# Optimization experiments

Hardware: AMD Instinct MI355X
Metric: run time of the kernel (lower is better)

Reference implementation:

```python
import jax, jax.numpy as jnp
import numpy as np

N_NODES = 50000
N_EDGES = 800000
F_IN = 11
HID = 128
N_ACT = 6


def _gcn_conv(x, W, b, src, dst, n):
    # PyG GCNConv: x' = D^{-1/2}(A+I)D^{-1/2} (x W) + b, with self-loops.
    h = x @ W  # [N, H]
    ones = jnp.ones(src.shape[0], dtype=h.dtype)
    deg = jax.ops.segment_sum(ones, dst, num_segments=n) + 1.0  # +1 self-loop
    dinv = jax.lax.rsqrt(deg)
    enorm = dinv[src] * dinv[dst]  # [E]
    msg = h[src] * enorm[:, None]  # gather + scale
    agg = jax.ops.segment_sum(msg, dst, num_segments=n)
    agg = agg + h * (dinv * dinv)[:, None]  # self-loop contribution (norm = 1/deg)
    return agg + b


def _mlp2(x, W1, b1, W2, b2):
    return jax.nn.relu(x @ W1 + b1) @ W2 + b2


def setup_inputs() -> dict:
    key = jax.random.key(0)
    ks = jax.random.split(key, 16)
    def g(k, shape, scale):
        return jax.random.normal(k, shape, dtype=jnp.float32) * scale
    x = g(ks[0], (N_NODES, F_IN), 1.0)
    edge_index = jax.random.randint(ks[1], (2, N_EDGES), 0, N_NODES, dtype=jnp.int64)
    return {
        "x": x,
        "edge_index": edge_index,
        "W1": g(ks[2], (F_IN, HID), 1.0 / np.sqrt(F_IN)),
        "b1": jnp.zeros((HID,), jnp.float32),
        "W2": g(ks[3], (HID, HID), 1.0 / np.sqrt(HID)),
        "b2": jnp.zeros((HID,), jnp.float32),
        "W3": g(ks[4], (HID, HID), 1.0 / np.sqrt(HID)),
        "b3": jnp.zeros((HID,), jnp.float32),
        "Wv1": g(ks[5], (HID, HID), 1.0 / np.sqrt(HID)),
        "bv1": jnp.zeros((HID,), jnp.float32),
        "Wv2": g(ks[6], (HID, 1), 1.0 / np.sqrt(HID)),
        "bv2": jnp.zeros((1,), jnp.float32),
        "Wa1": g(ks[7], (HID, HID), 1.0 / np.sqrt(HID)),
        "ba1": jnp.zeros((HID,), jnp.float32),
        "Wa2": g(ks[8], (HID, N_ACT), 1.0 / np.sqrt(HID)),
        "ba2": jnp.zeros((N_ACT,), jnp.float32),
    }


def reference(x, edge_index, W1, b1, W2, b2, W3, b3,
              Wv1, bv1, Wv2, bv2, Wa1, ba1, Wa2, ba2):
    src, dst = edge_index[0], edge_index[1]
    n = x.shape[0]
    h = jax.nn.relu(_gcn_conv(x, W1, b1, src, dst, n))
    h = jax.nn.relu(_gcn_conv(h, W2, b2, src, dst, n))
    h = jax.nn.relu(_gcn_conv(h, W3, b3, src, dst, n))
    # global_mean_pool with batch = zeros -> single-graph mean over nodes
    g = jnp.mean(h, axis=0, keepdims=True)  # [1, HID]
    value = _mlp2(g, Wv1, bv1, Wv2, bv2)          # [1, 1]
    advantage = _mlp2(g, Wa1, ba1, Wa2, ba2)      # [1, N_ACT]
    q = value + (advantage - jnp.mean(advantage, axis=-1, keepdims=True))
    return q
```

## Files before the change

kernel.cpp:

```cpp
#include <hip/hip_runtime.h>

#define HID 128
#define F_IN 11
#define FP 16
#define N_ACT 6
#define EPB 2048
#define LMAX 6144
#define CAP 8192

typedef __bf16 bf16;
typedef __bf16 v8bf __attribute__((ext_vector_type(8)));
typedef float f32x4 __attribute__((ext_vector_type(4)));
typedef float v2f __attribute__((ext_vector_type(2)));

__device__ inline float lo16(unsigned u) { return __uint_as_float(u << 16); }
__device__ inline float hi16(unsigned u) { return __uint_as_float(u & 0xffff0000u); }
__device__ inline unsigned pk2(float a, float b) {
  union { bf16 h; unsigned short u; } x, y;
  x.h = (bf16)a; y.h = (bf16)b;
  return ((unsigned)y.u << 16) | x.u;
}
__device__ inline v2f fp8_dec_lo(unsigned v) {
  return __builtin_amdgcn_cvt_pk_f32_fp8(v, false);
}
__device__ inline v2f fp8_dec_hi(unsigned v) {
  return __builtin_amdgcn_cvt_pk_f32_fp8(v, true);
}
__device__ inline unsigned fp8_enc2_lo(float a, float b, unsigned old) {
  return __builtin_amdgcn_cvt_pk_fp8_f32(a, b, old, false);
}
__device__ inline unsigned fp8_enc2_hi(float a, float b, unsigned old) {
  return __builtin_amdgcn_cvt_pk_fp8_f32(a, b, old, true);
}
__device__ inline unsigned char fp8_enc1(float v) {
  return (unsigned char)(__builtin_amdgcn_cvt_pk_fp8_f32(v, v, 0u, false) & 0xffu);
}


__global__ __launch_bounds__(256) void k_init(int* __restrict__ gcur,
                                              float* __restrict__ gsum, int nbkt) {
  int t = threadIdx.x;
  if (t < nbkt) gcur[t] = t * CAP;
  if (t < HID) gsum[t] = 0.f;
}

__global__ __launch_bounds__(256) void k_part(const int* __restrict__ esrc,
                                              const int* __restrict__ edst,
                                              int* __restrict__ gcur,
                                              unsigned* __restrict__ ebuf,
                                              const float* __restrict__ W2,
                                              const float* __restrict__ W3,
                                              bf16* __restrict__ WT2,
                                              bf16* __restrict__ WT3,
                                              int E, int nbkt) {
  __shared__ int hist[256], lofs[256], lcur[256], gbase[256];
  __shared__ unsigned sbuf[EPB];
  int t = threadIdx.x;
  hist[t] = 0;
  if (blockIdx.x < 64) {
    int i = blockIdx.x * 256 + t;
    int nn = i >> 7, k = i & 127;
    WT2[i] = (bf16)W2[k * 128 + nn];
    WT3[i] = (bf16)W3[k * 128 + nn];
  }
  __syncthreads();
  int start = blockIdx.x * EPB, end = min(E, start + EPB);
  unsigned u[8];
#pragma unroll
  for (int i = 0; i < 8; ++i) {
    int e = start + t + i * 256;
    if (e < end) {
      int s = esrc[e], d = edst[e];
      u[i] = ((unsigned)d << 16) | (unsigned)s;
      atomicAdd(&hist[d >> 8], 1);
    }
  }
  __syncthreads();
  int h = hist[t];
  lofs[t] = h;
  __syncthreads();
  for (int off = 1; off < 256; off <<= 1) {
    int x = (t >= off) ? lofs[t - off] : 0;
    __syncthreads();
    lofs[t] += x;
    __syncthreads();
  }
  lcur[t] = lofs[t] - h;
  if (t < nbkt && h) gbase[t] = atomicAdd(&gcur[t], h);
  __syncthreads();
#pragma unroll
  for (int i = 0; i < 8; ++i) {
    int e = start + t + i * 256;
    if (e < end) {
      int b = (int)(u[i] >> 24);
      int p = atomicAdd(&lcur[b], 1);
      sbuf[p] = u[i];
    }
  }
  __syncthreads();
  int m = end - start;
  for (int i = t; i < m; i += 256) {
    unsigned v = sbuf[i];
    int b = (int)(v >> 24);
    int excl = lofs[b] - hist[b];
    ebuf[gbase[b] + (i - excl)] = v;
  }
}

__global__ __launch_bounds__(256) void k_local(const unsigned* __restrict__ ebuf,
                                               const int* __restrict__ gcur,
                                               int2* __restrict__ rbe,
                                               float* __restrict__ dinv,
                                               unsigned short* __restrict__ cs,
                                               const float* __restrict__ x,
                                               bf16* __restrict__ xs, int n) {
  __shared__ int hist[256], lofs[256], cur[256];
  __shared__ float dsh[256];
  __shared__ unsigned sb[LMAX];
  int b = blockIdx.x, t = threadIdx.x;
  int rb = b * CAP, re = gcur[b];
  int m = re - rb;
  int nbase = b << 8;
  bool fit = (m <= LMAX);
  hist[t] = 0;
  __syncthreads();
  if (fit) {
    for (int i = t; i < m; i += 256) {
      unsigned u = ebuf[rb + i];
      sb[i] = u;
      atomicAdd(&hist[(int)(u >> 16) - nbase], 1);
    }
  } else {
    for (int i = t; i < m; i += 256)
      atomicAdd(&hist[(int)(ebuf[rb + i] >> 16) - nbase], 1);
  }
  __syncthreads();
  int h = hist[t];
  lofs[t] = h;
  __syncthreads();
  for (int off = 1; off < 256; off <<= 1) {
    int v = (t >= off) ? lofs[t - off] : 0;
    __syncthreads();
    lofs[t] += v;
    __syncthreads();
  }
  int excl = lofs[t] - h;
  cur[t] = rb + excl;
  float dv = rsqrtf((float)h + 1.0f);
  dsh[t] = dv;
  int g = nbase + t;
  if (g < n) {
    rbe[g] = make_int2(rb + excl, rb + lofs[t]);
    dinv[g] = dv;
  }
  __syncthreads();
  if (fit) {
    for (int i = t; i < m; i += 256) {
      unsigned u = sb[i];
      int p = atomicAdd(&cur[(int)(u >> 16) - nbase], 1);
      cs[p] = (unsigned short)(u & 0xffffu);
    }
  } else {
    for (int i = t; i < m; i += 256) {
      unsigned u = ebuf[rb + i];
      int p = atomicAdd(&cur[(int)(u >> 16) - nbase], 1);
      cs[p] = (unsigned short)(u & 0xffffu);
    }
  }
  for (int i = t; i < 256 * FP; i += 256) {
    int node = nbase + (i >> 4), c = i & 15;
    if (node < n)
      xs[(size_t)node * FP + c] =
          (bf16)((c < F_IN) ? x[(size_t)node * F_IN + c] * dsh[i >> 4] : 0.f);
  }
}


__global__ __launch_bounds__(256) void k_layer1(const bf16* __restrict__ xs,
                                                const float* __restrict__ dinv,
                                                const int2* __restrict__ rbe,
                                                const unsigned short* __restrict__ cs,
                                                const float* __restrict__ W1,
                                                const float* __restrict__ b1,
                                                unsigned* __restrict__ H8, int n) {
  __shared__ float Ws[F_IN * HID];
  __shared__ float A1s[64][17];
  int tid = threadIdx.x;
  int n0 = blockIdx.x * 64;
  for (int i = tid; i < F_IN * HID; i += 256) Ws[i] = W1[i];
  int wave = tid >> 6, lane = tid & 63;
  int g8 = lane >> 3, c = lane & 7;
  const unsigned* xs2 = (const unsigned*)xs;
#pragma unroll
  for (int r = 0; r < 2; ++r) {
    int row = wave * 16 + r * 8 + g8;
    int node = n0 + row;
    unsigned sv = 0;
    int j = 0, jend = 0;
    float dd = 0.f;
    if (node < n) {
      sv = xs2[(size_t)node * 8 + c];
      int2 be = rbe[node];
      j = be.x; jend = be.y;
      dd = dinv[node];
    }
    float ax = lo16(sv), ay = hi16(sv);
    for (; j < jend; j += 4) {
#pragma unroll
      for (int k = 0; k < 4; ++k) {
        int jj = j + k;
        bool ok = jj < jend;
        int sidx = cs[ok ? jj : jend - 1];
        unsigned v = xs2[(size_t)sidx * 8 + c];
        float mm = ok ? 1.f : 0.f;
        ax = fmaf(lo16(v), mm, ax);
        ay = fmaf(hi16(v), mm, ay);
      }
    }
    A1s[row][c * 2] = ax * dd;
    A1s[row][c * 2 + 1] = ay * dd;
  }
  __syncthreads();
  int tc = tid & 15, tr = tid >> 4;
  float bb[8];
#pragma unroll
  for (int j = 0; j < 8; ++j) bb[j] = b1[tc * 8 + j];
#pragma unroll
  for (int i = 0; i < 4; ++i) {
    int row = tr * 4 + i;
    int node = n0 + row;
    if (node >= n) continue;
    float acc[8];
#pragma unroll
    for (int j = 0; j < 8; ++j) acc[j] = 0.f;
#pragma unroll
    for (int k = 0; k < F_IN; ++k) {
      float xk = A1s[row][k];
      const float* wr = &Ws[k * HID + tc * 8];
#pragma unroll
      for (int j = 0; j < 8; ++j) acc[j] = fmaf(xk, wr[j], acc[j]);
    }
    float dd = dinv[node];
    float o[8];
#pragma unroll
    for (int j = 0; j < 8; ++j) o[j] = fmaxf(acc[j] + bb[j], 0.f) * dd;
    unsigned w0 = 0, w1 = 0;
    w0 = fp8_enc2_lo(o[0], o[1], w0);
    w0 = fp8_enc2_hi(o[2], o[3], w0);
    w1 = fp8_enc2_lo(o[4], o[5], w1);
    w1 = fp8_enc2_hi(o[6], o[7], w1);
    ((uint2*)H8)[(size_t)node * 16 + tc] = make_uint2(w0, w1);
  }
}


__global__ __launch_bounds__(256) void k_gather(const unsigned* __restrict__ tab,
                                                const float* __restrict__ dinv,
                                                const int2* __restrict__ rbe,
                                                const unsigned short* __restrict__ cs,
                                                bf16* __restrict__ A, int n, int nbx) {
  int bid = blockIdx.x;
  int slice = bid / nbx;
  int bx = bid - slice * nbx;
  int t = threadIdx.x;
  int node = bx * 16 + (t >> 4);
  int c = t & 15;
  int soff = slice * 16;
  if (node >= n) return;
  unsigned sv = tab[(size_t)node * 32 + soff + c];
  v2f slo = fp8_dec_lo(sv), shi = fp8_dec_hi(sv);
  float a0 = slo.x, a1 = slo.y, a2 = shi.x, a3 = shi.y;
  int2 be = rbe[node];
  int j = be.x, jend = be.y;
  for (; j < jend; j += 8) {
#pragma unroll
    for (int k = 0; k < 8; ++k) {
      int jj = j + k;
      bool ok = jj < jend;
      int sidx = cs[ok ? jj : jend - 1];
      unsigned v = tab[(size_t)sidx * 32 + soff + c];
      float mm = ok ? 1.f : 0.f;
      v2f lo = fp8_dec_lo(v), hi = fp8_dec_hi(v);
      a0 = fmaf(lo.x, mm, a0);
      a1 = fmaf(lo.y, mm, a1);
      a2 = fmaf(hi.x, mm, a2);
      a3 = fmaf(hi.y, mm, a3);
    }
  }
  float dd = dinv[node];
  ((uint2*)A)[(size_t)node * 32 + slice * 16 + c] =
      make_uint2(pk2(a0 * dd, a1 * dd), pk2(a2 * dd, a3 * dd));
}


__global__ __launch_bounds__(256) void k_gemm_mfma(const bf16* __restrict__ A,
                                                   const bf16* __restrict__ WT,
                                                   const float* __restrict__ b,
                                                   const float* __restrict__ dinv,
                                                   unsigned char* __restrict__ H8, int n) {
  __shared__ bf16 Asm[64 * 128];
  __shared__ bf16 Wsm[128 * 128];
  int tid = threadIdx.x;
  int n0 = blockIdx.x * 64;
  {
    float4* As4 = (float4*)Asm;
#pragma unroll
    for (int it = 0; it < 4; ++it) {
      int i = tid + it * 256;
      int row = i >> 4, kc = i & 15;
      float4 v = make_float4(0.f, 0.f, 0.f, 0.f);
      if (n0 + row < n) v = ((const float4*)(A + (size_t)(n0 + row) * 128))[kc];
      As4[row * 16 + (kc ^ (row & 7))] = v;
    }
    const float4* Wg = (const float4*)WT;
    float4* Ws4 = (float4*)Wsm;
#pragma unroll
    for (int it = 0; it < 8; ++it) {
      int i = tid + it * 256;
      int row = i >> 4, kc = i & 15;
      Ws4[row * 16 + (kc ^ (row & 7))] = Wg[i];
    }
  }
  __syncthreads();
  int lane = tid & 63, wave = tid >> 6;
  int l15 = lane & 15, g = lane >> 4;
  f32x4 acc[8];
#pragma unroll
  for (int f = 0; f < 8; ++f) acc[f] = (f32x4){0.f, 0.f, 0.f, 0.f};
  int arow = wave * 16 + l15;
  const float4* As4 = (const float4*)Asm;
  const float4* Ws4 = (const float4*)Wsm;
#pragma unroll
  for (int kk = 0; kk < 4; ++kk) {
    int kc = kk * 4 + g;
    v8bf a = *(const v8bf*)&As4[arow * 16 + (kc ^ (arow & 7))];
#pragma unroll
    for (int f = 0; f < 8; ++f) {
      int nrow = f * 16 + l15;
      v8bf bf = *(const v8bf*)&Ws4[nrow * 16 + (kc ^ (nrow & 7))];
      acc[f] = __builtin_amdgcn_mfma_f32_16x16x32_bf16(a, bf, acc[f], 0, 0, 0);
    }
  }
  int nodebase = n0 + wave * 16 + g * 4;
  float dv[4];
#pragma unroll
  for (int j = 0; j < 4; ++j)
    dv[j] = (nodebase + j < n) ? dinv[nodebase + j] : 1.f;
#pragma unroll
  for (int f = 0; f < 8; ++f) {
    float bias = b[f * 16 + l15];
#pragma unroll
    for (int j = 0; j < 4; ++j) {
      int node = nodebase + j;
      if (node < n) {
        float v = fmaxf(acc[f][j] + bias, 0.f) * dv[j];
        H8[(size_t)node * 128 + f * 16 + l15] = fp8_enc1(v);
      }
    }
  }
}

__global__ __launch_bounds__(256) void k_gemm_mfma3(const bf16* __restrict__ A,
                                                    const bf16* __restrict__ WT,
                                                    const float* __restrict__ b,
                                                    float* __restrict__ gsum, int n) {
  __shared__ bf16 Asm[64 * 128];
  __shared__ bf16 Wsm[128 * 128];
  __shared__ float colacc[128];
  int tid = threadIdx.x;
  int n0 = blockIdx.x * 64;
  if (tid < 128) colacc[tid] = 0.f;
  {
    float4* As4 = (float4*)Asm;
#pragma unroll
    for (int it = 0; it < 4; ++it) {
      int i = tid + it * 256;
      int row = i >> 4, kc = i & 15;
      float4 v = make_float4(0.f, 0.f, 0.f, 0.f);
      if (n0 + row < n) v = ((const float4*)(A + (size_t)(n0 + row) * 128))[kc];
      As4[row * 16 + (kc ^ (row & 7))] = v;
    }
    const float4* Wg = (const float4*)WT;
    float4* Ws4 = (float4*)Wsm;
#pragma unroll
    for (int it = 0; it < 8; ++it) {
      int i = tid + it * 256;
      int row = i >> 4, kc = i & 15;
      Ws4[row * 16 + (kc ^ (row & 7))] = Wg[i];
    }
  }
  __syncthreads();
  int lane = tid & 63, wave = tid >> 6;
  int l15 = lane & 15, g = lane >> 4;
  f32x4 acc[8];
#pragma unroll
  for (int f = 0; f < 8; ++f) acc[f] = (f32x4){0.f, 0.f, 0.f, 0.f};
  int arow = wave * 16 + l15;
  const float4* As4 = (const float4*)Asm;
  const float4* Ws4 = (const float4*)Wsm;
#pragma unroll
  for (int kk = 0; kk < 4; ++kk) {
    int kc = kk * 4 + g;
    v8bf a = *(const v8bf*)&As4[arow * 16 + (kc ^ (arow & 7))];
#pragma unroll
    for (int f = 0; f < 8; ++f) {
      int nrow = f * 16 + l15;
      v8bf bf = *(const v8bf*)&Ws4[nrow * 16 + (kc ^ (nrow & 7))];
      acc[f] = __builtin_amdgcn_mfma_f32_16x16x32_bf16(a, bf, acc[f], 0, 0, 0);
    }
  }
  int nodebase = n0 + wave * 16 + g * 4;
#pragma unroll
  for (int f = 0; f < 8; ++f) {
    float bias = b[f * 16 + l15];
    float sf = 0.f;
#pragma unroll
    for (int j = 0; j < 4; ++j) {
      int node = nodebase + j;
      if (node < n) sf += fmaxf(acc[f][j] + bias, 0.f);
    }
    atomicAdd(&colacc[f * 16 + l15], sf);
  }
  __syncthreads();
  if (tid < 128) atomicAdd(&gsum[tid], colacc[tid]);
}


__global__ __launch_bounds__(128) void k_head(const float* __restrict__ gsum,
    const float* __restrict__ Wv1, const float* __restrict__ bv1,
    const float* __restrict__ Wv2, const float* __restrict__ bv2,
    const float* __restrict__ Wa1, const float* __restrict__ ba1,
    const float* __restrict__ Wa2, const float* __restrict__ ba2,
    float* __restrict__ out, int n) {
  __shared__ float gs[HID], ha[HID], red[2], advs[N_ACT], vsh;
  int t = threadIdx.x;
  gs[t] = gsum[t] * (1.0f / (float)n);
  __syncthreads();
  float av = bv1[t], aa = ba1[t];
  for (int k = 0; k < HID; ++k) {
    float gk = gs[k];
    av = fmaf(gk, Wv1[k * HID + t], av);
    aa = fmaf(gk, Wa1[k * HID + t], aa);
  }
  float hv = fmaxf(av, 0.f);
  ha[t] = fmaxf(aa, 0.f);
  float pv = hv * Wv2[t];
#pragma unroll
  for (int o = 32; o > 0; o >>= 1) pv += __shfl_down(pv, o);
  if ((t & 63) == 0) red[t >> 6] = pv;
  __syncthreads();
  if (t == 0) vsh = red[0] + red[1] + bv2[0];
  if (t < N_ACT) {
    float adv = ba2[t];
    for (int j = 0; j < HID; ++j) adv = fmaf(ha[j], Wa2[j * N_ACT + t], adv);
    advs[t] = adv;
  }
  __syncthreads();
  if (t < N_ACT) {
    float m = 0.f;
#pragma unroll
    for (int a = 0; a < N_ACT; ++a) m += advs[a];
    m *= (1.0f / N_ACT);
    out[t] = vsh + advs[t] - m;
  }
}


extern "C" void kernel_launch(void* const* d_in, const int* in_sizes, int n_in,
                              void* d_out, int out_size, void* d_ws, size_t ws_size,
                              hipStream_t stream) {
  const float* x   = (const float*)d_in[0];
  const int*   ei  = (const int*)d_in[1];
  const float* W1  = (const float*)d_in[2];
  const float* b1  = (const float*)d_in[3];
  const float* W2  = (const float*)d_in[4];
  const float* b2  = (const float*)d_in[5];
  const float* W3  = (const float*)d_in[6];
  const float* b3  = (const float*)d_in[7];
  const float* Wv1 = (const float*)d_in[8];
  const float* bv1 = (const float*)d_in[9];
  const float* Wv2 = (const float*)d_in[10];
  const float* bv2 = (const float*)d_in[11];
  const float* Wa1 = (const float*)d_in[12];
  const float* ba1 = (const float*)d_in[13];
  const float* Wa2 = (const float*)d_in[14];
  const float* ba2 = (const float*)d_in[15];
  float* out = (float*)d_out;

  const int N = in_sizes[0] / F_IN;
  const int E = in_sizes[1] / 2;
  const int* esrc = ei;
  const int* edst = ei + E;
  const int nbkt = (N + 255) >> 8;
  const int gE = (E + EPB - 1) / EPB;

  char* p = (char*)d_ws;
  auto alloc = [&](size_t bytes) {
    void* r = (void*)p;
    p += (bytes + 1023) & ~(size_t)1023;
    return r;
  };
  unsigned* ebuf   = (unsigned*)alloc((size_t)nbkt * CAP * 4);
  int*   gcur      = (int*)alloc((size_t)nbkt * 4);
  int2*  rbe       = (int2*)alloc((size_t)N * 8);
  float* dinv      = (float*)alloc((size_t)N * 4);
  unsigned short* cs = (unsigned short*)alloc((size_t)nbkt * CAP * 2);
  bf16*  xs        = (bf16*)alloc((size_t)N * FP * 2);
  bf16*  WT2       = (bf16*)alloc(128 * 128 * 2);
  bf16*  WT3       = (bf16*)alloc(128 * 128 * 2);
  unsigned* H8a    = (unsigned*)alloc((size_t)N * 128);
  unsigned* H8b    = (unsigned*)alloc((size_t)N * 128);
  bf16*  A         = (bf16*)alloc((size_t)N * HID * 2);
  float* gsum      = (float*)alloc(HID * 4);

  k_init<<<1, 256, 0, stream>>>(gcur, gsum, nbkt);
  k_part<<<gE, 256, 0, stream>>>(esrc, edst, gcur, ebuf, W2, W3, WT2, WT3, E, nbkt);
  k_local<<<nbkt, 256, 0, stream>>>(ebuf, gcur, rbe, dinv, cs, x, xs, N);

  k_layer1<<<(N + 63) / 64, 256, 0, stream>>>(xs, dinv, rbe, cs, W1, b1, H8a, N);

  const int nbx = (N + 15) / 16;
  k_gather<<<nbx * 2, 256, 0, stream>>>(H8a, dinv, rbe, cs, A, N, nbx);
  k_gemm_mfma<<<(N + 63) / 64, 256, 0, stream>>>(A, WT2, b2, dinv, (unsigned char*)H8b, N);
  k_gather<<<nbx * 2, 256, 0, stream>>>(H8b, dinv, rbe, cs, A, N, nbx);
  k_gemm_mfma3<<<(N + 63) / 64, 256, 0, stream>>>(A, WT3, b3, gsum, N);

  k_head<<<1, 128, 0, stream>>>(gsum, Wv1, bv1, Wv2, bv2, Wa1, ba1, Wa2, ba2, out, N);
}
```

Baseline: 157.4 us.

## Fuse neighbor gather into MFMA GEMM per layer and widen local sort blocks

Each 128-wide GCN layer's gather (sum of fp8 neighbor rows) now writes its bf16 result straight into shared memory of a 512-thread block, which then runs the MFMA GEMM. This removes the A intermediate round trip through global memory and two kernel launches. The weight matrix is no longer staged in LDS; B fragments are read directly from global/L2. The local bucket-sort kernel also moves to 1024 threads per block. In exchange, gather parallelism per block changes (one 32-lane half-wave per node instead of 16-lane slices), and direct global weight reads may add latency.

```diff
diff --git a/kernel.cpp b/kernel.cpp
--- a/kernel.cpp
+++ b/kernel.cpp
@@ -107,13 +107,13 @@
   }
 }
 
-__global__ __launch_bounds__(256) void k_local(const unsigned* __restrict__ ebuf,
-                                               const int* __restrict__ gcur,
-                                               int2* __restrict__ rbe,
-                                               float* __restrict__ dinv,
-                                               unsigned short* __restrict__ cs,
-                                               const float* __restrict__ x,
-                                               bf16* __restrict__ xs, int n) {
+__global__ __launch_bounds__(1024) void k_local(const unsigned* __restrict__ ebuf,
+                                                const int* __restrict__ gcur,
+                                                int2* __restrict__ rbe,
+                                                float* __restrict__ dinv,
+                                                unsigned short* __restrict__ cs,
+                                                const float* __restrict__ x,
+                                                bf16* __restrict__ xs, int n) {
   __shared__ int hist[256], lofs[256], cur[256];
   __shared__ float dsh[256];
   __shared__ unsigned sb[LMAX];
@@ -122,52 +122,54 @@
   int m = re - rb;
   int nbase = b << 8;
   bool fit = (m <= LMAX);
-  hist[t] = 0;
+  if (t < 256) hist[t] = 0;
   __syncthreads();
   if (fit) {
-    for (int i = t; i < m; i += 256) {
+    for (int i = t; i < m; i += 1024) {
       unsigned u = ebuf[rb + i];
       sb[i] = u;
       atomicAdd(&hist[(int)(u >> 16) - nbase], 1);
     }
   } else {
-    for (int i = t; i < m; i += 256)
+    for (int i = t; i < m; i += 1024)
       atomicAdd(&hist[(int)(ebuf[rb + i] >> 16) - nbase], 1);
   }
   __syncthreads();
-  int h = hist[t];
-  lofs[t] = h;
+  int h = 0;
+  if (t < 256) { h = hist[t]; lofs[t] = h; }
   __syncthreads();
   for (int off = 1; off < 256; off <<= 1) {
-    int v = (t >= off) ? lofs[t - off] : 0;
+    int v = (t < 256 && t >= off) ? lofs[t - off] : 0;
     __syncthreads();
-    lofs[t] += v;
+    if (t < 256) lofs[t] += v;
     __syncthreads();
   }
-  int excl = lofs[t] - h;
-  cur[t] = rb + excl;
-  float dv = rsqrtf((float)h + 1.0f);
-  dsh[t] = dv;
-  int g = nbase + t;
-  if (g < n) {
-    rbe[g] = make_int2(rb + excl, rb + lofs[t]);
-    dinv[g] = dv;
+  if (t < 256) {
+    int excl = lofs[t] - h;
+    cur[t] = rb + excl;
+    float dv = rsqrtf((float)h + 1.0f);
+    dsh[t] = dv;
+    int g = nbase + t;
+    if (g < n) {
+      rbe[g] = make_int2(rb + excl, rb + lofs[t]);
+      dinv[g] = dv;
+    }
   }
   __syncthreads();
   if (fit) {
-    for (int i = t; i < m; i += 256) {
+    for (int i = t; i < m; i += 1024) {
       unsigned u = sb[i];
       int p = atomicAdd(&cur[(int)(u >> 16) - nbase], 1);
       cs[p] = (unsigned short)(u & 0xffffu);
     }
   } else {
-    for (int i = t; i < m; i += 256) {
+    for (int i = t; i < m; i += 1024) {
       unsigned u = ebuf[rb + i];
       int p = atomicAdd(&cur[(int)(u >> 16) - nbase], 1);
       cs[p] = (unsigned short)(u & 0xffffu);
     }
   }
-  for (int i = t; i < 256 * FP; i += 256) {
+  for (int i = t; i < 256 * FP; i += 1024) {
     int node = nbase + (i >> 4), c = i & 15;
     if (node < n)
       xs[(size_t)node * FP + c] =
@@ -254,175 +256,110 @@
 }
 
 
-__global__ __launch_bounds__(256) void k_gather(const unsigned* __restrict__ tab,
-                                                const float* __restrict__ dinv,
-                                                const int2* __restrict__ rbe,
-                                                const unsigned short* __restrict__ cs,
-                                                bf16* __restrict__ A, int n, int nbx) {
-  int bid = blockIdx.x;
-  int slice = bid / nbx;
-  int bx = bid - slice * nbx;
-  int t = threadIdx.x;
-  int node = bx * 16 + (t >> 4);
-  int c = t & 15;
-  int soff = slice * 16;
-  if (node >= n) return;
-  unsigned sv = tab[(size_t)node * 32 + soff + c];
-  v2f slo = fp8_dec_lo(sv), shi = fp8_dec_hi(sv);
-  float a0 = slo.x, a1 = slo.y, a2 = shi.x, a3 = shi.y;
-  int2 be = rbe[node];
-  int j = be.x, jend = be.y;
-  for (; j < jend; j += 8) {
-#pragma unroll
-    for (int k = 0; k < 8; ++k) {
-      int jj = j + k;
-      bool ok = jj < jend;
-      int sidx = cs[ok ? jj : jend - 1];
-      unsigned v = tab[(size_t)sidx * 32 + soff + c];
-      float mm = ok ? 1.f : 0.f;
-      v2f lo = fp8_dec_lo(v), hi = fp8_dec_hi(v);
-      a0 = fmaf(lo.x, mm, a0);
-      a1 = fmaf(lo.y, mm, a1);
-      a2 = fmaf(hi.x, mm, a2);
-      a3 = fmaf(hi.y, mm, a3);
-    }
-  }
-  float dd = dinv[node];
-  ((uint2*)A)[(size_t)node * 32 + slice * 16 + c] =
-      make_uint2(pk2(a0 * dd, a1 * dd), pk2(a2 * dd, a3 * dd));
-}
-
-
-__global__ __launch_bounds__(256) void k_gemm_mfma(const bf16* __restrict__ A,
-                                                   const bf16* __restrict__ WT,
-                                                   const float* __restrict__ b,
-                                                   const float* __restrict__ dinv,
-                                                   unsigned char* __restrict__ H8, int n) {
+template <bool FINAL>
+__global__ __launch_bounds__(512) void k_layer(const unsigned* __restrict__ tab,
+                                               const float* __restrict__ dinv,
+                                               const int2* __restrict__ rbe,
+                                               const unsigned short* __restrict__ cs,
+                                               const bf16* __restrict__ WT,
+                                               const float* __restrict__ b,
+                                               unsigned char* __restrict__ H8,
+                                               float* __restrict__ gsum, int n) {
   __shared__ bf16 Asm[64 * 128];
-  __shared__ bf16 Wsm[128 * 128];
-  int tid = threadIdx.x;
-  int n0 = blockIdx.x * 64;
-  {
-    float4* As4 = (float4*)Asm;
-#pragma unroll
-    for (int it = 0; it < 4; ++it) {
-      int i = tid + it * 256;
-      int row = i >> 4, kc = i & 15;
-      float4 v = make_float4(0.f, 0.f, 0.f, 0.f);
-      if (n0 + row < n) v = ((const float4*)(A + (size_t)(n0 + row) * 128))[kc];
-      As4[row * 16 + (kc ^ (row & 7))] = v;
-    }
-    const float4* Wg = (const float4*)WT;
-    float4* Ws4 = (float4*)Wsm;
-#pragma unroll
-    for (int it = 0; it < 8; ++it) {
-      int i = tid + it * 256;
-      int row = i >> 4, kc = i & 15;
-      Ws4[row * 16 + (kc ^ (row & 7))] = Wg[i];
-    }
-  }
-  __syncthreads();
-  int lane = tid & 63, wave = tid >> 6;
-  int l15 = lane & 15, g = lane >> 4;
-  f32x4 acc[8];
-#pragma unroll
-  for (int f = 0; f < 8; ++f) acc[f] = (f32x4){0.f, 0.f, 0.f, 0.f};
-  int arow = wave * 16 + l15;
-  const float4* As4 = (const float4*)Asm;
-  const float4* Ws4 = (const float4*)Wsm;
-#pragma unroll
-  for (int kk = 0; kk < 4; ++kk) {
-    int kc = kk * 4 + g;
-    v8bf a = *(const v8bf*)&As4[arow * 16 + (kc ^ (arow & 7))];
-#pragma unroll
-    for (int f = 0; f < 8; ++f) {
-      int nrow = f * 16 + l15;
-      v8bf bf = *(const v8bf*)&Ws4[nrow * 16 + (kc ^ (nrow & 7))];
-      acc[f] = __builtin_amdgcn_mfma_f32_16x16x32_bf16(a, bf, acc[f], 0, 0, 0);
-    }
-  }
-  int nodebase = n0 + wave * 16 + g * 4;
-  float dv[4];
-#pragma unroll
-  for (int j = 0; j < 4; ++j)
-    dv[j] = (nodebase + j < n) ? dinv[nodebase + j] : 1.f;
-#pragma unroll
-  for (int f = 0; f < 8; ++f) {
-    float bias = b[f * 16 + l15];
-#pragma unroll
-    for (int j = 0; j < 4; ++j) {
-      int node = nodebase + j;
-      if (node < n) {
-        float v = fmaxf(acc[f][j] + bias, 0.f) * dv[j];
-        H8[(size_t)node * 128 + f * 16 + l15] = fp8_enc1(v);
-      }
-    }
-  }
-}
-
-__global__ __launch_bounds__(256) void k_gemm_mfma3(const bf16* __restrict__ A,
-                                                    const bf16* __restrict__ WT,
-                                                    const float* __restrict__ b,
-                                                    float* __restrict__ gsum, int n) {
-  __shared__ bf16 Asm[64 * 128];
-  __shared__ bf16 Wsm[128 * 128];
   __shared__ float colacc[128];
   int tid = threadIdx.x;
   int n0 = blockIdx.x * 64;
-  if (tid < 128) colacc[tid] = 0.f;
-  {
-    float4* As4 = (float4*)Asm;
-#pragma unroll
-    for (int it = 0; it < 4; ++it) {
-      int i = tid + it * 256;
-      int row = i >> 4, kc = i & 15;
-      float4 v = make_float4(0.f, 0.f, 0.f, 0.f);
-      if (n0 + row < n) v = ((const float4*)(A + (size_t)(n0 + row) * 128))[kc];
-      As4[row * 16 + (kc ^ (row & 7))] = v;
-    }
-    const float4* Wg = (const float4*)WT;
-    float4* Ws4 = (float4*)Wsm;
-#pragma unroll
-    for (int it = 0; it < 8; ++it) {
-      int i = tid + it * 256;
-      int row = i >> 4, kc = i & 15;
-      Ws4[row * 16 + (kc ^ (row & 7))] = Wg[i];
-    }
-  }
-  __syncthreads();
-  int lane = tid & 63, wave = tid >> 6;
+  if (FINAL && tid < 128) colacc[tid] = 0.f;
+  int wave = tid >> 6, lane = tid & 63;
+  int sub = lane >> 5;
+  int c = lane & 31;
+#pragma unroll
+  for (int r = 0; r < 4; ++r) {
+    int row = wave * 8 + r * 2 + sub;
+    int node = n0 + row;
+    float a0 = 0.f, a1 = 0.f, a2 = 0.f, a3 = 0.f, dd = 0.f;
+    int j = 0, jend = 0;
+    if (node < n) {
+      unsigned sv = tab[(size_t)node * 32 + c];
+      v2f lo = fp8_dec_lo(sv), hi = fp8_dec_hi(sv);
+      a0 = lo.x; a1 = lo.y; a2 = hi.x; a3 = hi.y;
+      int2 be = rbe[node];
+      j = be.x; jend = be.y;
+      dd = dinv[node];
+    }
+    for (; j < jend; j += 8) {
+#pragma unroll
+      for (int k = 0; k < 8; ++k) {
+        int jj = j + k;
+        bool ok = jj < jend;
+        int sidx = cs[ok ? jj : jend - 1];
+        unsigned v = tab[(size_t)sidx * 32 + c];
+        float mm = ok ? 1.f : 0.f;
+        v2f lo = fp8_dec_lo(v), hi = fp8_dec_hi(v);
+        a0 = fmaf(lo.x, mm, a0);
+        a1 = fmaf(lo.y, mm, a1);
+        a2 = fmaf(hi.x, mm, a2);
+        a3 = fmaf(hi.y, mm, a3);
+      }
+    }
+    int kc = c >> 1, half = c & 1;
+    uint2 w = make_uint2(pk2(a0 * dd, a1 * dd), pk2(a2 * dd, a3 * dd));
+    *(uint2*)((char*)Asm + row * 256 + ((kc ^ (row & 7)) << 4) + (half << 3)) = w;
+  }
+  __syncthreads();
   int l15 = lane & 15, g = lane >> 4;
-  f32x4 acc[8];
-#pragma unroll
-  for (int f = 0; f < 8; ++f) acc[f] = (f32x4){0.f, 0.f, 0.f, 0.f};
-  int arow = wave * 16 + l15;
-  const float4* As4 = (const float4*)Asm;
-  const float4* Ws4 = (const float4*)Wsm;
+  int rg = (wave & 3) * 16;
+  int cg = (wave >> 2) * 64;
+  f32x4 acc[4];
+#pragma unroll
+  for (int f = 0; f < 4; ++f) acc[f] = (f32x4){0.f, 0.f, 0.f, 0.f};
+  int arow = rg + l15;
 #pragma unroll
   for (int kk = 0; kk < 4; ++kk) {
     int kc = kk * 4 + g;
-    v8bf a = *(const v8bf*)&As4[arow * 16 + (kc ^ (arow & 7))];
-#pragma unroll
-    for (int f = 0; f < 8; ++f) {
-      int nrow = f * 16 + l15;
-      v8bf bf = *(const v8bf*)&Ws4[nrow * 16 + (kc ^ (nrow & 7))];
-      acc[f] = __builtin_amdgcn_mfma_f32_16x16x32_bf16(a, bf, acc[f], 0, 0, 0);
-    }
-  }
-  int nodebase = n0 + wave * 16 + g * 4;
-#pragma unroll
-  for (int f = 0; f < 8; ++f) {
-    float bias = b[f * 16 + l15];
-    float sf = 0.f;
-#pragma unroll
-    for (int j = 0; j < 4; ++j) {
-      int node = nodebase + j;
-      if (node < n) sf += fmaxf(acc[f][j] + bias, 0.f);
-    }
-    atomicAdd(&colacc[f * 16 + l15], sf);
-  }
-  __syncthreads();
-  if (tid < 128) atomicAdd(&gsum[tid], colacc[tid]);
+    v8bf a = *(const v8bf*)((const char*)Asm + arow * 256 + ((kc ^ (arow & 7)) << 4));
+#pragma unroll
+    for (int f = 0; f < 4; ++f) {
+      int nrow = cg + f * 16 + l15;
+      v8bf bfr = *(const v8bf*)(WT + (size_t)nrow * 128 + kc * 8);
+      acc[f] = __builtin_amdgcn_mfma_f32_16x16x32_bf16(a, bfr, acc[f], 0, 0, 0);
+    }
+  }
+  int nodebase = n0 + rg + g * 4;
+  if (FINAL) {
+#pragma unroll
+    for (int f = 0; f < 4; ++f) {
+      int col = cg + f * 16 + l15;
+      float bias = b[col];
+      float sf = 0.f;
+#pragma unroll
+      for (int j = 0; j < 4; ++j) {
+        int node = nodebase + j;
+        if (node < n) sf += fmaxf(acc[f][j] + bias, 0.f);
+      }
+      atomicAdd(&colacc[col], sf);
+    }
+    __syncthreads();
+    if (tid < 128) atomicAdd(&gsum[tid], colacc[tid]);
+  } else {
+    float dv[4];
+#pragma unroll
+    for (int j = 0; j < 4; ++j)
+      dv[j] = (nodebase + j < n) ? dinv[nodebase + j] : 1.f;
+#pragma unroll
+    for (int f = 0; f < 4; ++f) {
+      int col = cg + f * 16 + l15;
+      float bias = b[col];
+#pragma unroll
+      for (int j = 0; j < 4; ++j) {
+        int node = nodebase + j;
+        if (node < n) {
+          float v = fmaxf(acc[f][j] + bias, 0.f) * dv[j];
+          H8[(size_t)node * 128 + col] = fp8_enc1(v);
+        }
+      }
+    }
+  }
 }
 
 
@@ -510,20 +447,19 @@
   bf16*  WT3       = (bf16*)alloc(128 * 128 * 2);
   unsigned* H8a    = (unsigned*)alloc((size_t)N * 128);
   unsigned* H8b    = (unsigned*)alloc((size_t)N * 128);
-  bf16*  A         = (bf16*)alloc((size_t)N * HID * 2);
   float* gsum      = (float*)alloc(HID * 4);
 
   k_init<<<1, 256, 0, stream>>>(gcur, gsum, nbkt);
   k_part<<<gE, 256, 0, stream>>>(esrc, edst, gcur, ebuf, W2, W3, WT2, WT3, E, nbkt);
-  k_local<<<nbkt, 256, 0, stream>>>(ebuf, gcur, rbe, dinv, cs, x, xs, N);
+  k_local<<<nbkt, 1024, 0, stream>>>(ebuf, gcur, rbe, dinv, cs, x, xs, N);
 
   k_layer1<<<(N + 63) / 64, 256, 0, stream>>>(xs, dinv, rbe, cs, W1, b1, H8a, N);
 
-  const int nbx = (N + 15) / 16;
-  k_gather<<<nbx * 2, 256, 0, stream>>>(H8a, dinv, rbe, cs, A, N, nbx);
-  k_gemm_mfma<<<(N + 63) / 64, 256, 0, stream>>>(A, WT2, b2, dinv, (unsigned char*)H8b, N);
-  k_gather<<<nbx * 2, 256, 0, stream>>>(H8b, dinv, rbe, cs, A, N, nbx);
-  k_gemm_mfma3<<<(N + 63) / 64, 256, 0, stream>>>(A, WT3, b3, gsum, N);
+  int gL = (N + 63) / 64;
+  k_layer<false><<<gL, 512, 0, stream>>>(H8a, dinv, rbe, cs, WT2, b2,
+                                         (unsigned char*)H8b, gsum, N);
+  k_layer<true><<<gL, 512, 0, stream>>>(H8b, dinv, rbe, cs, WT3, b3,
+                                        (unsigned char*)nullptr, gsum, N);
 
   k_head<<<1, 128, 0, stream>>>(gsum, Wv1, bv1, Wv2, bv2, Wa1, ba1, Wa2, ba2, out, N);
 }
```

Result: faster. 146.9 us (-6.7%).
